# Optimization experiments

Measured on AMD Instinct MI355X. Metric: run time of the kernel, lower is better.

Reference implementation:

```python
import jax, jax.numpy as jnp
import numpy as np

N = 100000   # nodes
E = 600000   # edges
D = 128      # input = hidden = output dim
L = 3        # GNN layers
C = 40       # num_classes
EPS = 1e-5   # BatchNorm eps


def setup_inputs() -> dict:
    key = jax.random.key(0)
    ks = jax.random.split(key, 8)
    x = jax.random.normal(ks[0], (N, D), jnp.float32)
    edge_index = jax.random.randint(ks[1], (2, E), 0, N, jnp.int32)
    # GCNConv weights per layer (Glorot-ish scale), bias zeros
    Ws = jax.random.normal(ks[2], (L, D, D), jnp.float32) / np.sqrt(D)
    bs = jnp.zeros((L, D), jnp.float32)
    # BatchNorm affine params
    gammas = jnp.ones((L, D), jnp.float32)
    betas = jnp.zeros((L, D), jnp.float32)
    # PReLU single slope per layer (torch default init 0.25)
    prelu_a = jnp.full((L,), 0.25, jnp.float32)
    # classification head: Linear(D,D) -> ReLU -> Linear(D,C)
    Wh1 = jax.random.normal(ks[3], (D, D), jnp.float32) / np.sqrt(D)
    bh1 = jnp.zeros((D,), jnp.float32)
    Wh2 = jax.random.normal(ks[4], (D, C), jnp.float32) / np.sqrt(D)
    bh2 = jnp.zeros((C,), jnp.float32)
    return dict(x=x, edge_index=edge_index, Ws=Ws, bs=bs, gammas=gammas,
                betas=betas, prelu_a=prelu_a, Wh1=Wh1, bh1=bh1, Wh2=Wh2, bh2=bh2)


def _gcn_conv(h, src, dst, norm, W, b):
    # PyG GCNConv: out_i = sum_{j->i} norm_ij * (x_j W) + b  (self-loops already in src/dst)
    m = (h @ W)[src] * norm[:, None]          # [E+N, D_out]
    return jax.ops.segment_sum(m, dst, num_segments=N) + b


def reference(x, edge_index, Ws, bs, gammas, betas, prelu_a, Wh1, bh1, Wh2, bh2):
    # add self-loops + symmetric normalization (computed once; same graph each layer)
    loops = jnp.arange(N, dtype=edge_index.dtype)
    src = jnp.concatenate([edge_index[0], loops])
    dst = jnp.concatenate([edge_index[1], loops])
    deg = jax.ops.segment_sum(jnp.ones_like(dst, jnp.float32), dst, num_segments=N)
    dinv = jax.lax.rsqrt(jnp.maximum(deg, 1.0))  # deg >= 1 thanks to self-loops
    norm = dinv[src] * dinv[dst]                 # [E+N]

    h = x
    for l in range(L):
        h = _gcn_conv(h, src, dst, norm, Ws[l], bs[l])
        # BatchNorm in training mode: batch statistics over nodes
        mu = h.mean(axis=0)
        var = h.var(axis=0)
        h = (h - mu) * jax.lax.rsqrt(var + EPS) * gammas[l] + betas[l]
        # PReLU
        h = jnp.where(h > 0, h, prelu_a[l] * h)

    embeddings = h
    logits = jax.nn.relu(embeddings @ Wh1 + bh1) @ Wh2 + bh2
    out = jnp.argmax(logits, axis=1)
    return embeddings, logits, out
```

## Files before the change

### kernel.cpp

```cpp
#include <hip/hip_runtime.h>
#include <hip/hip_bf16.h>
#include <cstddef>

#define N_NODES 100000
#define N_EDGES 600000
#define DD 128
#define LL 3
#define CC 40
#define BN_EPS 1e-5f

typedef __attribute__((ext_vector_type(8))) short bfrag;
typedef __attribute__((ext_vector_type(4))) float f32x4;

__device__ __forceinline__ float ldf(const void* p, long i, int f32) {
    return f32 ? ((const float*)p)[i] : __bfloat162float(((const __hip_bfloat16*)p)[i]);
}
__device__ __forceinline__ void stf(void* p, long i, float v, int f32) {
    if (f32) ((float*)p)[i] = v;
    else     ((__hip_bfloat16*)p)[i] = __float2bfloat16(v);
}

__device__ __forceinline__ unsigned short f2bf(float f) {
    unsigned u = __float_as_uint(f);
    unsigned r = (u + 0x7fffu + ((u >> 16) & 1u)) >> 16;
    return (unsigned short)r;
}
__device__ __forceinline__ float bf2f(unsigned short h) {
    return __uint_as_float(((unsigned)h) << 16);
}

__global__ __launch_bounds__(256) void k_detect(const void* __restrict__ x, int* __restrict__ dflag) {
    __shared__ int s[256];
    int t = threadIdx.x;
    const __hip_bfloat16* xb = (const __hip_bfloat16*)x;
    int bad = 0;
    for (int i = t; i < 4096; i += 256) {
        float v = __bfloat162float(xb[i]);
        float a = fabsf(v);
        if (!(a < 1e6f)) bad++;
        else if (v != 0.f && a < 1e-30f) bad++;
    }
    s[t] = bad; __syncthreads();
    for (int off = 128; off > 0; off >>= 1) {
        if (t < off) s[t] += s[t + off];
        __syncthreads();
    }
    if (t == 0) *dflag = (s[0] > 64) ? 1 : 0;
}

__global__ __launch_bounds__(256) void k_packw(const void* __restrict__ Ws, const void* __restrict__ Wh1,
                                               unsigned short* __restrict__ Wp,
                                               const int* __restrict__ dflag) {
    int f = *dflag;
    int u = blockIdx.x * 256 + threadIdx.x;
    int mat = u >> 14;
    int r = u & 16383;
    int k = r >> 7, c = r & 127;
    float wv = (mat < 3) ? ldf(Ws, (long)mat * 16384 + r, f) : ldf(Wh1, r, f);
    unsigned short hi = f2bf(wv);
    float r1 = wv - bf2f(hi);
    unsigned short mid = f2bf(r1);
    float r2 = r1 - bf2f(mid);
    unsigned short lo = f2bf(r2);
    int n = c >> 4, ks = k >> 5, j = k & 7;
    int lanep = (c & 15) | (((k >> 3) & 3) << 4);
    long base = (long)mat * 49152 + (long)((n * 4 + ks) * 3) * 512 + lanep * 8 + j;
    Wp[base] = hi;
    Wp[base + 512] = mid;
    Wp[base + 1024] = lo;
}


__global__ __launch_bounds__(256) void k_init(int* cnt, int* fpos, int* rowptr, float* stats) {
    int i = blockIdx.x * 256 + threadIdx.x;
    if (i < N_NODES) { cnt[i] = 0; fpos[i] = 0; }
    if (i < 6 * DD) stats[i] = 0.f;
    if (i == 0) rowptr[N_NODES] = N_EDGES;
}

__global__ __launch_bounds__(256) void k_count(const int* __restrict__ ei, int* __restrict__ cnt) {
    int e = blockIdx.x * 256 + threadIdx.x;
    if (e < N_EDGES) atomicAdd(&cnt[ei[N_EDGES + e]], 1);
}

__global__ __launch_bounds__(256) void k_scan1(const int* __restrict__ cnt, int* __restrict__ rowptr,
                                               int* __restrict__ bsum, float* __restrict__ dinv) {
    __shared__ int s[256];
    int t = threadIdx.x;
    int i = blockIdx.x * 256 + t;
    int v = (i < N_NODES) ? cnt[i] : 0;
    if (i < N_NODES) dinv[i] = 1.f / sqrtf((float)(1 + v));
    s[t] = v; __syncthreads();
    for (int off = 1; off < 256; off <<= 1) {
        int x = (t >= off) ? s[t - off] : 0;
        __syncthreads();
        s[t] += x; __syncthreads();
    }
    if (i < N_NODES) rowptr[i] = s[t] - v;
    if (t == 255) bsum[blockIdx.x] = s[255];
}

__global__ __launch_bounds__(512) void k_scan2(int* bsum, int nb) {
    __shared__ int s[512];
    int t = threadIdx.x;
    int v = (t < nb) ? bsum[t] : 0;
    s[t] = v; __syncthreads();
    for (int off = 1; off < 512; off <<= 1) {
        int x = (t >= off) ? s[t - off] : 0;
        __syncthreads();
        s[t] += x; __syncthreads();
    }
    if (t < nb) bsum[t] = s[t] - v;
}

__global__ __launch_bounds__(256) void k_scan3(int* rowptr, const int* __restrict__ bsum) {
    int i = blockIdx.x * 256 + threadIdx.x;
    if (i < N_NODES) rowptr[i] += bsum[blockIdx.x];
}

__global__ __launch_bounds__(256) void k_fill(const int* __restrict__ ei, int* __restrict__ fpos,
                                              const int* __restrict__ rowptr, int* __restrict__ adj,
                                              float* __restrict__ wadj, const float* __restrict__ dinv) {
    int e = blockIdx.x * 256 + threadIdx.x;
    if (e < N_EDGES) {
        int s = ei[e];
        int d = ei[N_EDGES + e];
        int p = atomicAdd(&fpos[d], 1);
        int pos = rowptr[d] + p;
        adj[pos] = s;
        wadj[pos] = dinv[s];
    }
}

__device__ __forceinline__ float4 load_row4(const void* __restrict__ src, long row, int q, int f) {
    if (f) {
        return ((const float4*)src)[row * 32 + q];
    } else {
        uint2 u = ((const uint2*)src)[row * 32 + q];
        float4 v;
        v.x = __uint_as_float(u.x << 16);
        v.y = __uint_as_float(u.x & 0xffff0000u);
        v.z = __uint_as_float(u.y << 16);
        v.w = __uint_as_float(u.y & 0xffff0000u);
        return v;
    }
}


__global__ __launch_bounds__(256) void k_agg(const void* __restrict__ src,
                                             const int* __restrict__ rowptr,
                                             const int* __restrict__ adj,
                                             const float* __restrict__ wadj,
                                             const float* __restrict__ dinv,
                                             const float* __restrict__ bnp,
                                             float* __restrict__ outp,
                                             const int* __restrict__ dflag) {
    int f = *dflag;
    int lane = threadIdx.x & 63;
    int h = lane >> 5;
    int q = lane & 31;
    int i = blockIdx.x * 4 + (threadIdx.x >> 6);
    if (i >= N_NODES) return;

    float4 sc = make_float4(1.f, 1.f, 1.f, 1.f);
    float4 sh = make_float4(0.f, 0.f, 0.f, 0.f);
    float al = 0.f;
    bool useBN = (bnp != nullptr);
    if (useBN) {
        sc = ((const float4*)bnp)[q];
        sh = ((const float4*)(bnp + 128))[q];
        al = bnp[256];
    }

    float di = dinv[i];
    int e0 = rowptr[i], e1 = rowptr[i + 1];

    float a0 = 0.f, a1 = 0.f, a2 = 0.f, a3 = 0.f;
    if (h == 0) {
        float4 v = load_row4(src, i, q, f);
        if (useBN) {
            float y;
            y = fmaf(v.x, sc.x, sh.x); v.x = (y > 0.f) ? y : al * y;
            y = fmaf(v.y, sc.y, sh.y); v.y = (y > 0.f) ? y : al * y;
            y = fmaf(v.z, sc.z, sh.z); v.z = (y > 0.f) ? y : al * y;
            y = fmaf(v.w, sc.w, sh.w); v.w = (y > 0.f) ? y : al * y;
        }
        a0 = di * v.x; a1 = di * v.y; a2 = di * v.z; a3 = di * v.w;
    }

    for (int base = e0; base < e1; base += 64) {
        int m = e1 - base; if (m > 64) m = 64;
        int ajl = (lane < m) ? adj[base + lane] : 0;
        float wl = (lane < m) ? wadj[base + lane] : 0.f;
        for (int t = 0; t < m; t += 4) {
            int s0 = t + h;     if (s0 > 63) s0 = 63;
            int s1 = t + 2 + h; if (s1 > 63) s1 = 63;
            int j0 = __shfl(ajl, s0);
            int j1 = __shfl(ajl, s1);
            float w0 = __shfl(wl, s0);
            float w1 = __shfl(wl, s1);
            float4 v0 = load_row4(src, j0, q, f);
            float4 v1 = load_row4(src, j1, q, f);
            if (useBN) {
                float y;
                y = fmaf(v0.x, sc.x, sh.x); v0.x = (y > 0.f) ? y : al * y;
                y = fmaf(v0.y, sc.y, sh.y); v0.y = (y > 0.f) ? y : al * y;
                y = fmaf(v0.z, sc.z, sh.z); v0.z = (y > 0.f) ? y : al * y;
                y = fmaf(v0.w, sc.w, sh.w); v0.w = (y > 0.f) ? y : al * y;
                y = fmaf(v1.x, sc.x, sh.x); v1.x = (y > 0.f) ? y : al * y;
                y = fmaf(v1.y, sc.y, sh.y); v1.y = (y > 0.f) ? y : al * y;
                y = fmaf(v1.z, sc.z, sh.z); v1.z = (y > 0.f) ? y : al * y;
                y = fmaf(v1.w, sc.w, sh.w); v1.w = (y > 0.f) ? y : al * y;
            }
            a0 += w0 * v0.x + w1 * v1.x;
            a1 += w0 * v0.y + w1 * v1.y;
            a2 += w0 * v0.z + w1 * v1.z;
            a3 += w0 * v0.w + w1 * v1.w;
        }
    }

    a0 += __shfl_xor(a0, 32);
    a1 += __shfl_xor(a1, 32);
    a2 += __shfl_xor(a2, 32);
    a3 += __shfl_xor(a3, 32);

    if (h == 0) {
        float4 r = make_float4(di * a0, di * a1, di * a2, di * a3);
        ((float4*)outp)[(size_t)i * 32 + q] = r;
    }
}


__global__ __launch_bounds__(256, 2) void k_gemm2(const float* __restrict__ A,
                                                  const unsigned short* __restrict__ Wp,
                                                  const void* __restrict__ bias, long boff,
                                                  const float* __restrict__ bnpA,
                                                  float* __restrict__ stats,
                                                  float* __restrict__ Cout, int relu,
                                                  const int* __restrict__ dflag) {
    __shared__ unsigned short Wl[24576];
    int f = *dflag;
    int tid = threadIdx.x;

    int lane = tid & 63;
    int w = tid >> 6;
    int lr = lane & 15;
    int lg = lane >> 4;
    int rowbase = blockIdx.x * 128 + w * 32;

    float bcol[8];
    #pragma unroll
    for (int n = 0; n < 8; ++n)
        bcol[n] = bias ? ldf(bias, boff + n * 16 + lr, f) : 0.f;

    float alA = bnpA ? bnpA[256] : 0.f;

    bfrag ah[2][4], am[2][4], alo[2][4];
    const float4* A4 = (const float4*)A;
    #pragma unroll
    for (int ks = 0; ks < 4; ++ks) {
        int k0 = ks * 32 + lg * 8;
        float bs_[8], bh_[8];
        if (bnpA) {
            float4 sa = *(const float4*)&bnpA[k0];
            float4 sb = *(const float4*)&bnpA[k0 + 4];
            float4 ha = *(const float4*)&bnpA[128 + k0];
            float4 hb = *(const float4*)&bnpA[128 + k0 + 4];
            bs_[0] = sa.x; bs_[1] = sa.y; bs_[2] = sa.z; bs_[3] = sa.w;
            bs_[4] = sb.x; bs_[5] = sb.y; bs_[6] = sb.z; bs_[7] = sb.w;
            bh_[0] = ha.x; bh_[1] = ha.y; bh_[2] = ha.z; bh_[3] = ha.w;
            bh_[4] = hb.x; bh_[5] = hb.y; bh_[6] = hb.z; bh_[7] = hb.w;
        }
        #pragma unroll
        for (int s = 0; s < 2; ++s) {
            int row = rowbase + s * 16 + lr;
            float xv[8];
            if (row < N_NODES) {
                long bi = (long)row * 32 + (k0 >> 2);
                float4 x0 = A4[bi], x1 = A4[bi + 1];
                xv[0] = x0.x; xv[1] = x0.y; xv[2] = x0.z; xv[3] = x0.w;
                xv[4] = x1.x; xv[5] = x1.y; xv[6] = x1.z; xv[7] = x1.w;
            } else {
                #pragma unroll
                for (int e = 0; e < 8; ++e) xv[e] = 0.f;
            }
            if (bnpA) {
                #pragma unroll
                for (int e = 0; e < 8; ++e) {
                    float y = fmaf(xv[e], bs_[e], bh_[e]);
                    xv[e] = (y > 0.f) ? y : alA * y;
                }
            }
            bfrag hfr, mfr, lfr;
            #pragma unroll
            for (int e = 0; e < 8; ++e) {
                unsigned short hb2 = f2bf(xv[e]);
                float r1 = xv[e] - bf2f(hb2);
                unsigned short mb2 = f2bf(r1);
                float r2 = r1 - bf2f(mb2);
                hfr[e] = (short)hb2;
                mfr[e] = (short)mb2;
                lfr[e] = (short)f2bf(r2);
            }
            ah[s][ks] = hfr;
            am[s][ks] = mfr;
            alo[s][ks] = lfr;
        }
    }

    f32x4 acc[2][8];
    #pragma unroll
    for (int s = 0; s < 2; ++s)
        #pragma unroll
        for (int n = 0; n < 8; ++n) acc[s][n] = (f32x4){0.f, 0.f, 0.f, 0.f};

    #pragma unroll
    for (int h = 0; h < 2; ++h) {
        if (h) __syncthreads();
        {
            const uint4* srcp = (const uint4*)(Wp + (size_t)h * 24576);
            uint4* dstp = (uint4*)Wl;
            #pragma unroll
            for (int u = 0; u < 12; ++u) dstp[tid + 256 * u] = srcp[tid + 256 * u];
        }
        __syncthreads();

        #pragma unroll
        for (int nn = 0; nn < 4; ++nn) {
            int n = h * 4 + nn;
            bfrag bh[4], bm[4], bl[4];
            #pragma unroll
            for (int ks = 0; ks < 4; ++ks) {
                int base = ((nn * 4 + ks) * 3) * 512 + lane * 8;
                bh[ks] = *(const bfrag*)&Wl[base];
                bm[ks] = *(const bfrag*)&Wl[base + 512];
                bl[ks] = *(const bfrag*)&Wl[base + 1024];
            }
            #pragma unroll
            for (int ks = 0; ks < 4; ++ks) {
                #pragma unroll
                for (int s = 0; s < 2; ++s) {
                    acc[s][n] = __builtin_amdgcn_mfma_f32_16x16x32_bf16(ah[s][ks],  bh[ks], acc[s][n], 0, 0, 0);
                    acc[s][n] = __builtin_amdgcn_mfma_f32_16x16x32_bf16(am[s][ks],  bh[ks], acc[s][n], 0, 0, 0);
                    acc[s][n] = __builtin_amdgcn_mfma_f32_16x16x32_bf16(ah[s][ks],  bm[ks], acc[s][n], 0, 0, 0);
                    acc[s][n] = __builtin_amdgcn_mfma_f32_16x16x32_bf16(am[s][ks],  bm[ks], acc[s][n], 0, 0, 0);
                    acc[s][n] = __builtin_amdgcn_mfma_f32_16x16x32_bf16(alo[s][ks], bh[ks], acc[s][n], 0, 0, 0);
                    acc[s][n] = __builtin_amdgcn_mfma_f32_16x16x32_bf16(ah[s][ks],  bl[ks], acc[s][n], 0, 0, 0);
                }
            }
        }
    }

    int rowst[2][4]; bool rv[2][4];
    #pragma unroll
    for (int s = 0; s < 2; ++s)
        #pragma unroll
        for (int reg = 0; reg < 4; ++reg) {
            rowst[s][reg] = rowbase + s * 16 + lg * 4 + reg;
            rv[s][reg] = rowst[s][reg] < N_NODES;
        }

    float ls[8], lq[8];
    #pragma unroll
    for (int n = 0; n < 8; ++n) { ls[n] = 0.f; lq[n] = 0.f; }

    #pragma unroll
    for (int s = 0; s < 2; ++s)
        #pragma unroll
        for (int n = 0; n < 8; ++n) {
            int colb = n * 16 + lr;
            #pragma unroll
            for (int reg = 0; reg < 4; ++reg) {
                if (rv[s][reg]) {
                    float o = acc[s][n][reg] + bcol[n];
                    if (relu) o = fmaxf(o, 0.f);
                    Cout[(long)rowst[s][reg] * 128 + colb] = o;
                    ls[n] += o;
                    lq[n] += o * o;
                }
            }
        }

    if (stats) {
        #pragma unroll
        for (int n = 0; n < 8; ++n) {
            ls[n] += __shfl_xor(ls[n], 16);
            ls[n] += __shfl_xor(ls[n], 32);
            lq[n] += __shfl_xor(lq[n], 16);
            lq[n] += __shfl_xor(lq[n], 32);
        }
        __syncthreads();
        float* red = (float*)Wl;
        if (lane < 16) {
            #pragma unroll
            for (int n = 0; n < 8; ++n) {
                red[w * 256 + n * 16 + lane] = ls[n];
                red[w * 256 + 128 + n * 16 + lane] = lq[n];
            }
        }
        __syncthreads();
        float t = red[tid] + red[256 + tid] + red[512 + tid] + red[768 + tid];
        atomicAdd(&stats[tid], t);
    }
}

__global__ __launch_bounds__(128) void k_bnprep(const float* __restrict__ stats,
                                                const void* __restrict__ g, const void* __restrict__ b,
                                                const void* __restrict__ a, int l,
                                                float* __restrict__ bnp, const int* __restrict__ dflag) {
    int f = *dflag;
    int c = threadIdx.x;
    float mean = stats[c] / (float)N_NODES;
    float var = stats[128 + c] / (float)N_NODES - mean * mean;
    float inv = 1.f / sqrtf(var + BN_EPS);
    float s = ldf(g, (long)l * DD + c, f) * inv;
    bnp[c] = s;
    bnp[128 + c] = ldf(b, (long)l * DD + c, f) - mean * s;
    if (c == 0) bnp[256] = ldf(a, l, f);
}

__global__ __launch_bounds__(256) void k_emb(const float* __restrict__ H, const float* __restrict__ bnp,
                                             void* __restrict__ out, const int* __restrict__ dflag) {
    int f = *dflag;
    long idx = (long)blockIdx.x * 256 + threadIdx.x;
    int c = (int)(idx & 127);
    float al = bnp[256];
    float y = fmaf(H[idx], bnp[c], bnp[128 + c]);
    y = (y > 0.f) ? y : al * y;
    stf(out, idx, y, f);
}


__global__ __launch_bounds__(256) void k_head(const float* __restrict__ Hd, const void* __restrict__ W2,
                                              const void* __restrict__ b2,
                                              void* __restrict__ out_base,
                                              const int* __restrict__ dflag) {
    __shared__ float Wl[128][40];
    __shared__ float bl[40];
    __shared__ float rv[32][8];
    __shared__ int ri[32][8];
    int f = *dflag;
    int tid = threadIdx.x;
    for (int u = tid; u < 128 * 40; u += 256) Wl[u / 40][u % 40] = ldf(W2, u, f);
    if (tid < 40) bl[tid] = ldf(b2, tid, f);
    __syncthreads();
    int rl = tid >> 3, g = tid & 7;
    long r = (long)blockIdx.x * 32 + rl;
    float acc[5];
    #pragma unroll
    for (int j = 0; j < 5; ++j) acc[j] = bl[g * 5 + j];
    for (int k = 0; k < 128; ++k) {
        float h = Hd[r * 128 + k];
        #pragma unroll
        for (int j = 0; j < 5; ++j) acc[j] += h * Wl[k][g * 5 + j];
    }
    float best = acc[0]; int bi = 0;
    #pragma unroll
    for (int j = 1; j < 5; ++j)
        if (acc[j] > best) { best = acc[j]; bi = j; }
    const long LOG_OFF = (long)N_NODES * DD;
    const long ARG_OFF = (long)N_NODES * (DD + CC);
    #pragma unroll
    for (int j = 0; j < 5; ++j) stf(out_base, LOG_OFF + r * 40 + g * 5 + j, acc[j], f);
    rv[rl][g] = best; ri[rl][g] = g * 5 + bi;
    __syncthreads();
    if (tid < 32) {
        long row = (long)blockIdx.x * 32 + tid;
        float bb = rv[tid][0]; int bbi = ri[tid][0];
        #pragma unroll
        for (int g2 = 1; g2 < 8; ++g2)
            if (rv[tid][g2] > bb) { bb = rv[tid][g2]; bbi = ri[tid][g2]; }
        stf(out_base, ARG_OFF + row, (float)bbi, f);
    }
}


extern "C" void kernel_launch(void* const* d_in, const int* in_sizes, int n_in,
                              void* d_out, int out_size, void* d_ws, size_t ws_size,
                              hipStream_t stream) {
    const void* x   = d_in[0];
    const int* ei   = (const int*)d_in[1];
    const void* Ws  = d_in[2];
    const void* bs  = d_in[3];
    const void* gam = d_in[4];
    const void* bet = d_in[5];
    const void* pa  = d_in[6];
    const void* Wh1 = d_in[7];
    const void* bh1 = d_in[8];
    const void* Wh2 = d_in[9];
    const void* bh2 = d_in[10];

    char* w = (char*)d_ws;
    int* cnt     = (int*)w;    w += sizeof(int) * N_NODES;
    int* fpos    = (int*)w;    w += sizeof(int) * N_NODES;
    int* rowptr  = (int*)w;    w += sizeof(int) * (N_NODES + 4);
    int* adj     = (int*)w;    w += sizeof(int) * N_EDGES;
    float* wadj  = (float*)w;  w += sizeof(float) * N_EDGES;
    int* bsum    = (int*)w;    w += sizeof(int) * 512;
    int* dflag   = (int*)w;    w += sizeof(int) * 4;
    float* dinv  = (float*)w;  w += sizeof(float) * N_NODES;
    float* stats = (float*)w;  w += sizeof(float) * (6 * DD);
    float* bnp   = (float*)w;  w += sizeof(float) * (3 * 512);
    unsigned short* Wp = (unsigned short*)w; w += sizeof(unsigned short) * 4 * 49152;
    float* bufA  = (float*)w;  w += sizeof(float) * (size_t)N_NODES * DD;
    float* bufB  = (float*)w;  w += sizeof(float) * (size_t)N_NODES * DD;

    const int scanBlocks = (N_NODES + 255) / 256;
    const int edgeBlocks = (N_EDGES + 255) / 256;
    const int elemBlocks = (N_NODES * DD) / 256;
    const int gemmBlocks = (N_NODES + 127) / 128;
    const int aggBlocks  = (N_NODES + 3) / 4;

    k_detect<<<1, 256, 0, stream>>>(x, dflag);
    k_packw<<<256, 256, 0, stream>>>(Ws, Wh1, Wp, dflag);
    k_init<<<scanBlocks, 256, 0, stream>>>(cnt, fpos, rowptr, stats);
    k_count<<<edgeBlocks, 256, 0, stream>>>(ei, cnt);
    k_scan1<<<scanBlocks, 256, 0, stream>>>(cnt, rowptr, bsum, dinv);
    k_scan2<<<1, 512, 0, stream>>>(bsum, scanBlocks);
    k_scan3<<<scanBlocks, 256, 0, stream>>>(rowptr, bsum);
    k_fill<<<edgeBlocks, 256, 0, stream>>>(ei, fpos, rowptr, adj, wadj, dinv);

    for (int l = 0; l < LL; ++l) {
        const void* src = (l == 0) ? x : (const void*)bufB;
        const float* bn = (l == 0) ? nullptr : (bnp + (l - 1) * 512);
        k_agg<<<aggBlocks, 256, 0, stream>>>(src, rowptr, adj, wadj, dinv, bn, bufA, dflag);
        k_gemm2<<<gemmBlocks, 256, 0, stream>>>(bufA, Wp + (size_t)l * 49152, bs, (long)l * DD,
                                                nullptr, stats + l * 256, bufB, 0, dflag);
        k_bnprep<<<1, 128, 0, stream>>>(stats + l * 256, gam, bet, pa, l, bnp + l * 512, dflag);
    }

    k_emb<<<elemBlocks, 256, 0, stream>>>(bufB, bnp + 2 * 512, d_out, dflag);
    k_gemm2<<<gemmBlocks, 256, 0, stream>>>(bufB, Wp + (size_t)3 * 49152, bh1, 0, bnp + 2 * 512,
                                            nullptr, bufA, 1, dflag);
    k_head<<<(N_NODES / 32), 256, 0, stream>>>(bufA, Wh2, bh2, d_out, dflag);
}
```

Measured before the change: 646.2 us.

## Fuse BN prep and embedding write into consumers, interleave adjacency, async weight loads

Removes the k_bnprep and k_emb kernels. BN scale and shift are now recomputed from the stats inside k_agg and k_gemm2, and the embedding output is written from the head GEMM's A-load path. Adjacency indices and weights are interleaved into one int2 array, and the aggregation inner loop is unrolled to four neighbor rows per step for more loads in flight. GEMM weight tiles are loaded with global_load_lds directly into LDS, and the first half is issued before the A-fragment setup. In exchange, every block redoes the per-channel sqrt and division work and carries more register pressure.

New measurement: 641.7 us. No clear change (-0.7%).

```diff
diff --git a/kernel.cpp b/kernel.cpp
--- a/kernel.cpp
+++ b/kernel.cpp
@@ -27,6 +27,11 @@
 }
 __device__ __forceinline__ float bf2f(unsigned short h) {
     return __uint_as_float(((unsigned)h) << 16);
+}
+
+__device__ __forceinline__ void gload_lds16(const unsigned short* g, unsigned short* l) {
+    __builtin_amdgcn_global_load_lds((const __attribute__((address_space(1))) unsigned int*)g,
+                                     (__attribute__((address_space(3))) unsigned int*)l, 16, 0, 0);
 }
 
 __global__ __launch_bounds__(256) void k_detect(const void* __restrict__ x, int* __restrict__ dflag) {
@@ -119,16 +124,14 @@
 }
 
 __global__ __launch_bounds__(256) void k_fill(const int* __restrict__ ei, int* __restrict__ fpos,
-                                              const int* __restrict__ rowptr, int* __restrict__ adj,
-                                              float* __restrict__ wadj, const float* __restrict__ dinv) {
+                                              const int* __restrict__ rowptr, int2* __restrict__ adjw,
+                                              const float* __restrict__ dinv) {
     int e = blockIdx.x * 256 + threadIdx.x;
     if (e < N_EDGES) {
         int s = ei[e];
         int d = ei[N_EDGES + e];
         int p = atomicAdd(&fpos[d], 1);
-        int pos = rowptr[d] + p;
-        adj[pos] = s;
-        wadj[pos] = dinv[s];
+        adjw[rowptr[d] + p] = make_int2(s, __float_as_int(dinv[s]));
     }
 }
 
@@ -146,13 +149,25 @@
     }
 }
 
+__device__ __forceinline__ float4 bn4(float4 v, float4 sc, float4 sh, float al) {
+    float y;
+    y = fmaf(v.x, sc.x, sh.x); v.x = (y > 0.f) ? y : al * y;
+    y = fmaf(v.y, sc.y, sh.y); v.y = (y > 0.f) ? y : al * y;
+    y = fmaf(v.z, sc.z, sh.z); v.z = (y > 0.f) ? y : al * y;
+    y = fmaf(v.w, sc.w, sh.w); v.w = (y > 0.f) ? y : al * y;
+    return v;
+}
+
 
 __global__ __launch_bounds__(256) void k_agg(const void* __restrict__ src,
                                              const int* __restrict__ rowptr,
-                                             const int* __restrict__ adj,
-                                             const float* __restrict__ wadj,
+                                             const int2* __restrict__ adjw,
                                              const float* __restrict__ dinv,
-                                             const float* __restrict__ bnp,
+                                             const float* __restrict__ stats,
+                                             const void* __restrict__ gam,
+                                             const void* __restrict__ bet,
+                                             const void* __restrict__ pa,
+                                             int bnl,
                                              float* __restrict__ outp,
                                              const int* __restrict__ dflag) {
     int f = *dflag;
@@ -162,14 +177,25 @@
     int i = blockIdx.x * 4 + (threadIdx.x >> 6);
     if (i >= N_NODES) return;
 
+    bool useBN = (stats != nullptr);
     float4 sc = make_float4(1.f, 1.f, 1.f, 1.f);
     float4 sh = make_float4(0.f, 0.f, 0.f, 0.f);
     float al = 0.f;
-    bool useBN = (bnp != nullptr);
     if (useBN) {
-        sc = ((const float4*)bnp)[q];
-        sh = ((const float4*)(bnp + 128))[q];
-        al = bnp[256];
+        const float invn = 1.f / (float)N_NODES;
+        float4 sm = ((const float4*)stats)[q];
+        float4 sq = ((const float4*)(stats + 128))[q];
+        long gb = (long)bnl * DD + 4 * q;
+        float m0 = sm.x * invn, m1 = sm.y * invn, m2 = sm.z * invn, m3 = sm.w * invn;
+        sc.x = ldf(gam, gb + 0, f) / sqrtf(sq.x * invn - m0 * m0 + BN_EPS);
+        sc.y = ldf(gam, gb + 1, f) / sqrtf(sq.y * invn - m1 * m1 + BN_EPS);
+        sc.z = ldf(gam, gb + 2, f) / sqrtf(sq.z * invn - m2 * m2 + BN_EPS);
+        sc.w = ldf(gam, gb + 3, f) / sqrtf(sq.w * invn - m3 * m3 + BN_EPS);
+        sh.x = ldf(bet, gb + 0, f) - m0 * sc.x;
+        sh.y = ldf(bet, gb + 1, f) - m1 * sc.y;
+        sh.z = ldf(bet, gb + 2, f) - m2 * sc.z;
+        sh.w = ldf(bet, gb + 3, f) - m3 * sc.w;
+        al = ldf(pa, bnl, f);
     }
 
     float di = dinv[i];
@@ -178,44 +204,37 @@
     float a0 = 0.f, a1 = 0.f, a2 = 0.f, a3 = 0.f;
     if (h == 0) {
         float4 v = load_row4(src, i, q, f);
-        if (useBN) {
-            float y;
-            y = fmaf(v.x, sc.x, sh.x); v.x = (y > 0.f) ? y : al * y;
-            y = fmaf(v.y, sc.y, sh.y); v.y = (y > 0.f) ? y : al * y;
-            y = fmaf(v.z, sc.z, sh.z); v.z = (y > 0.f) ? y : al * y;
-            y = fmaf(v.w, sc.w, sh.w); v.w = (y > 0.f) ? y : al * y;
-        }
+        if (useBN) v = bn4(v, sc, sh, al);
         a0 = di * v.x; a1 = di * v.y; a2 = di * v.z; a3 = di * v.w;
     }
 
     for (int base = e0; base < e1; base += 64) {
         int m = e1 - base; if (m > 64) m = 64;
-        int ajl = (lane < m) ? adj[base + lane] : 0;
-        float wl = (lane < m) ? wadj[base + lane] : 0.f;
-        for (int t = 0; t < m; t += 4) {
-            int s0 = t + h;     if (s0 > 63) s0 = 63;
-            int s1 = t + 2 + h; if (s1 > 63) s1 = 63;
-            int j0 = __shfl(ajl, s0);
-            int j1 = __shfl(ajl, s1);
-            float w0 = __shfl(wl, s0);
-            float w1 = __shfl(wl, s1);
-            float4 v0 = load_row4(src, j0, q, f);
-            float4 v1 = load_row4(src, j1, q, f);
+        int2 aw = (lane < m) ? adjw[base + lane] : make_int2(0, 0);
+        int ajl = aw.x;
+        float wl = __int_as_float(aw.y);
+        for (int t = 0; t < m; t += 8) {
+            int jj[4]; float ww[4];
+            #pragma unroll
+            for (int u = 0; u < 4; ++u) {
+                int s = t + 2 * u + h; if (s > 63) s = 63;
+                jj[u] = __shfl(ajl, s);
+                ww[u] = __shfl(wl, s);
+            }
+            float4 v0 = load_row4(src, jj[0], q, f);
+            float4 v1 = load_row4(src, jj[1], q, f);
+            float4 v2 = load_row4(src, jj[2], q, f);
+            float4 v3 = load_row4(src, jj[3], q, f);
             if (useBN) {
-                float y;
-                y = fmaf(v0.x, sc.x, sh.x); v0.x = (y > 0.f) ? y : al * y;
-                y = fmaf(v0.y, sc.y, sh.y); v0.y = (y > 0.f) ? y : al * y;
-                y = fmaf(v0.z, sc.z, sh.z); v0.z = (y > 0.f) ? y : al * y;
-                y = fmaf(v0.w, sc.w, sh.w); v0.w = (y > 0.f) ? y : al * y;
-                y = fmaf(v1.x, sc.x, sh.x); v1.x = (y > 0.f) ? y : al * y;
-                y = fmaf(v1.y, sc.y, sh.y); v1.y = (y > 0.f) ? y : al * y;
-                y = fmaf(v1.z, sc.z, sh.z); v1.z = (y > 0.f) ? y : al * y;
-                y = fmaf(v1.w, sc.w, sh.w); v1.w = (y > 0.f) ? y : al * y;
-            }
-            a0 += w0 * v0.x + w1 * v1.x;
-            a1 += w0 * v0.y + w1 * v1.y;
-            a2 += w0 * v0.z + w1 * v1.z;
-            a3 += w0 * v0.w + w1 * v1.w;
+                v0 = bn4(v0, sc, sh, al);
+                v1 = bn4(v1, sc, sh, al);
+                v2 = bn4(v2, sc, sh, al);
+                v3 = bn4(v3, sc, sh, al);
+            }
+            a0 += ww[0] * v0.x + ww[1] * v1.x + ww[2] * v2.x + ww[3] * v3.x;
+            a1 += ww[0] * v0.y + ww[1] * v1.y + ww[2] * v2.y + ww[3] * v3.y;
+            a2 += ww[0] * v0.z + ww[1] * v1.z + ww[2] * v2.z + ww[3] * v3.z;
+            a3 += ww[0] * v0.w + ww[1] * v1.w + ww[2] * v2.w + ww[3] * v3.w;
         }
     }
 
@@ -234,16 +253,26 @@
 __global__ __launch_bounds__(256, 2) void k_gemm2(const float* __restrict__ A,
                                                   const unsigned short* __restrict__ Wp,
                                                   const void* __restrict__ bias, long boff,
-                                                  const float* __restrict__ bnpA,
+                                                  const float* __restrict__ statsA,
+                                                  const void* __restrict__ gam,
+                                                  const void* __restrict__ bet,
+                                                  const void* __restrict__ pa, int bnl,
                                                   float* __restrict__ stats,
-                                                  float* __restrict__ Cout, int relu,
+                                                  float* __restrict__ Cout,
+                                                  void* __restrict__ embp, int relu,
                                                   const int* __restrict__ dflag) {
     __shared__ unsigned short Wl[24576];
     int f = *dflag;
     int tid = threadIdx.x;
-
     int lane = tid & 63;
     int w = tid >> 6;
+
+    #pragma unroll
+    for (int u = 0; u < 12; ++u) {
+        int chunk = w * 12 + u;
+        gload_lds16(Wp + chunk * 512 + lane * 8, &Wl[chunk * 512]);
+    }
+
     int lr = lane & 15;
     int lg = lane >> 4;
     int rowbase = blockIdx.x * 128 + w * 32;
@@ -253,7 +282,8 @@
     for (int n = 0; n < 8; ++n)
         bcol[n] = bias ? ldf(bias, boff + n * 16 + lr, f) : 0.f;
 
-    float alA = bnpA ? bnpA[256] : 0.f;
+    float alA = statsA ? ldf(pa, bnl, f) : 0.f;
+    const float invn = 1.f / (float)N_NODES;
 
     bfrag ah[2][4], am[2][4], alo[2][4];
     const float4* A4 = (const float4*)A;
@@ -261,15 +291,16 @@
     for (int ks = 0; ks < 4; ++ks) {
         int k0 = ks * 32 + lg * 8;
         float bs_[8], bh_[8];
-        if (bnpA) {
-            float4 sa = *(const float4*)&bnpA[k0];
-            float4 sb = *(const float4*)&bnpA[k0 + 4];
-            float4 ha = *(const float4*)&bnpA[128 + k0];
-            float4 hb = *(const float4*)&bnpA[128 + k0 + 4];
-            bs_[0] = sa.x; bs_[1] = sa.y; bs_[2] = sa.z; bs_[3] = sa.w;
-            bs_[4] = sb.x; bs_[5] = sb.y; bs_[6] = sb.z; bs_[7] = sb.w;
-            bh_[0] = ha.x; bh_[1] = ha.y; bh_[2] = ha.z; bh_[3] = ha.w;
-            bh_[4] = hb.x; bh_[5] = hb.y; bh_[6] = hb.z; bh_[7] = hb.w;
+        if (statsA) {
+            #pragma unroll
+            for (int e = 0; e < 8; ++e) {
+                int c = k0 + e;
+                float mean = statsA[c] * invn;
+                float varv = statsA[128 + c] * invn - mean * mean;
+                float s = ldf(gam, (long)bnl * DD + c, f) / sqrtf(varv + BN_EPS);
+                bs_[e] = s;
+                bh_[e] = ldf(bet, (long)bnl * DD + c, f) - mean * s;
+            }
         }
         #pragma unroll
         for (int s = 0; s < 2; ++s) {
@@ -284,7 +315,7 @@
                 #pragma unroll
                 for (int e = 0; e < 8; ++e) xv[e] = 0.f;
             }
-            if (bnpA) {
+            if (statsA) {
                 #pragma unroll
                 for (int e = 0; e < 8; ++e) {
                     float y = fmaf(xv[e], bs_[e], bh_[e]);
@@ -305,6 +336,19 @@
             ah[s][ks] = hfr;
             am[s][ks] = mfr;
             alo[s][ks] = lfr;
+            if (embp && row < N_NODES) {
+                if (f) {
+                    ((float4*)embp)[(long)row * 32 + (k0 >> 2)]     = make_float4(xv[0], xv[1], xv[2], xv[3]);
+                    ((float4*)embp)[(long)row * 32 + (k0 >> 2) + 1] = make_float4(xv[4], xv[5], xv[6], xv[7]);
+                } else {
+                    uint4 pk;
+                    pk.x = (unsigned)(unsigned short)hfr[0] | ((unsigned)(unsigned short)hfr[1] << 16);
+                    pk.y = (unsigned)(unsigned short)hfr[2] | ((unsigned)(unsigned short)hfr[3] << 16);
+                    pk.z = (unsigned)(unsigned short)hfr[4] | ((unsigned)(unsigned short)hfr[5] << 16);
+                    pk.w = (unsigned)(unsigned short)hfr[6] | ((unsigned)(unsigned short)hfr[7] << 16);
+                    ((uint4*)embp)[(long)row * 16 + (k0 >> 3)] = pk;
+                }
+            }
         }
     }
 
@@ -314,39 +358,62 @@
         #pragma unroll
         for (int n = 0; n < 8; ++n) acc[s][n] = (f32x4){0.f, 0.f, 0.f, 0.f};
 
-    #pragma unroll
-    for (int h = 0; h < 2; ++h) {
-        if (h) __syncthreads();
-        {
-            const uint4* srcp = (const uint4*)(Wp + (size_t)h * 24576);
-            uint4* dstp = (uint4*)Wl;
-            #pragma unroll
-            for (int u = 0; u < 12; ++u) dstp[tid + 256 * u] = srcp[tid + 256 * u];
-        }
-        __syncthreads();
-
-        #pragma unroll
-        for (int nn = 0; nn < 4; ++nn) {
-            int n = h * 4 + nn;
-            bfrag bh[4], bm[4], bl[4];
-            #pragma unroll
-            for (int ks = 0; ks < 4; ++ks) {
-                int base = ((nn * 4 + ks) * 3) * 512 + lane * 8;
-                bh[ks] = *(const bfrag*)&Wl[base];
-                bm[ks] = *(const bfrag*)&Wl[base + 512];
-                bl[ks] = *(const bfrag*)&Wl[base + 1024];
-            }
-            #pragma unroll
-            for (int ks = 0; ks < 4; ++ks) {
-                #pragma unroll
-                for (int s = 0; s < 2; ++s) {
-                    acc[s][n] = __builtin_amdgcn_mfma_f32_16x16x32_bf16(ah[s][ks],  bh[ks], acc[s][n], 0, 0, 0);
-                    acc[s][n] = __builtin_amdgcn_mfma_f32_16x16x32_bf16(am[s][ks],  bh[ks], acc[s][n], 0, 0, 0);
-                    acc[s][n] = __builtin_amdgcn_mfma_f32_16x16x32_bf16(ah[s][ks],  bm[ks], acc[s][n], 0, 0, 0);
-                    acc[s][n] = __builtin_amdgcn_mfma_f32_16x16x32_bf16(am[s][ks],  bm[ks], acc[s][n], 0, 0, 0);
-                    acc[s][n] = __builtin_amdgcn_mfma_f32_16x16x32_bf16(alo[s][ks], bh[ks], acc[s][n], 0, 0, 0);
-                    acc[s][n] = __builtin_amdgcn_mfma_f32_16x16x32_bf16(ah[s][ks],  bl[ks], acc[s][n], 0, 0, 0);
-                }
+    __syncthreads();
+
+    #pragma unroll
+    for (int nn = 0; nn < 4; ++nn) {
+        int n = nn;
+        bfrag bh[4], bm[4], bl[4];
+        #pragma unroll
+        for (int ks = 0; ks < 4; ++ks) {
+            int base = ((nn * 4 + ks) * 3) * 512 + lane * 8;
+            bh[ks] = *(const bfrag*)&Wl[base];
+            bm[ks] = *(const bfrag*)&Wl[base + 512];
+            bl[ks] = *(const bfrag*)&Wl[base + 1024];
+        }
+        #pragma unroll
+        for (int ks = 0; ks < 4; ++ks) {
+            #pragma unroll
+            for (int s = 0; s < 2; ++s) {
+                acc[s][n] = __builtin_amdgcn_mfma_f32_16x16x32_bf16(ah[s][ks],  bh[ks], acc[s][n], 0, 0, 0);
+                acc[s][n] = __builtin_amdgcn_mfma_f32_16x16x32_bf16(am[s][ks],  bh[ks], acc[s][n], 0, 0, 0);
+                acc[s][n] = __builtin_amdgcn_mfma_f32_16x16x32_bf16(ah[s][ks],  bm[ks], acc[s][n], 0, 0, 0);
+                acc[s][n] = __builtin_amdgcn_mfma_f32_16x16x32_bf16(am[s][ks],  bm[ks], acc[s][n], 0, 0, 0);
+                acc[s][n] = __builtin_amdgcn_mfma_f32_16x16x32_bf16(alo[s][ks], bh[ks], acc[s][n], 0, 0, 0);
+                acc[s][n] = __builtin_amdgcn_mfma_f32_16x16x32_bf16(ah[s][ks],  bl[ks], acc[s][n], 0, 0, 0);
+            }
+        }
+    }
+
+    __syncthreads();
+    #pragma unroll
+    for (int u = 0; u < 12; ++u) {
+        int chunk = w * 12 + u;
+        gload_lds16(Wp + 24576 + chunk * 512 + lane * 8, &Wl[chunk * 512]);
+    }
+    __syncthreads();
+
+    #pragma unroll
+    for (int nn = 0; nn < 4; ++nn) {
+        int n = 4 + nn;
+        bfrag bh[4], bm[4], bl[4];
+        #pragma unroll
+        for (int ks = 0; ks < 4; ++ks) {
+            int base = ((nn * 4 + ks) * 3) * 512 + lane * 8;
+            bh[ks] = *(const bfrag*)&Wl[base];
+            bm[ks] = *(const bfrag*)&Wl[base + 512];
+            bl[ks] = *(const bfrag*)&Wl[base + 1024];
+        }
+        #pragma unroll
+        for (int ks = 0; ks < 4; ++ks) {
+            #pragma unroll
+            for (int s = 0; s < 2; ++s) {
+                acc[s][n] = __builtin_amdgcn_mfma_f32_16x16x32_bf16(ah[s][ks],  bh[ks], acc[s][n], 0, 0, 0);
+                acc[s][n] = __builtin_amdgcn_mfma_f32_16x16x32_bf16(am[s][ks],  bh[ks], acc[s][n], 0, 0, 0);
+                acc[s][n] = __builtin_amdgcn_mfma_f32_16x16x32_bf16(ah[s][ks],  bm[ks], acc[s][n], 0, 0, 0);
+                acc[s][n] = __builtin_amdgcn_mfma_f32_16x16x32_bf16(am[s][ks],  bm[ks], acc[s][n], 0, 0, 0);
+                acc[s][n] = __builtin_amdgcn_mfma_f32_16x16x32_bf16(alo[s][ks], bh[ks], acc[s][n], 0, 0, 0);
+                acc[s][n] = __builtin_amdgcn_mfma_f32_16x16x32_bf16(ah[s][ks],  bl[ks], acc[s][n], 0, 0, 0);
             }
         }
     }
@@ -402,32 +469,6 @@
         float t = red[tid] + red[256 + tid] + red[512 + tid] + red[768 + tid];
         atomicAdd(&stats[tid], t);
     }
-}
-
-__global__ __launch_bounds__(128) void k_bnprep(const float* __restrict__ stats,
-                                                const void* __restrict__ g, const void* __restrict__ b,
-                                                const void* __restrict__ a, int l,
-                                                float* __restrict__ bnp, const int* __restrict__ dflag) {
-    int f = *dflag;
-    int c = threadIdx.x;
-    float mean = stats[c] / (float)N_NODES;
-    float var = stats[128 + c] / (float)N_NODES - mean * mean;
-    float inv = 1.f / sqrtf(var + BN_EPS);
-    float s = ldf(g, (long)l * DD + c, f) * inv;
-    bnp[c] = s;
-    bnp[128 + c] = ldf(b, (long)l * DD + c, f) - mean * s;
-    if (c == 0) bnp[256] = ldf(a, l, f);
-}
-
-__global__ __launch_bounds__(256) void k_emb(const float* __restrict__ H, const float* __restrict__ bnp,
-                                             void* __restrict__ out, const int* __restrict__ dflag) {
-    int f = *dflag;
-    long idx = (long)blockIdx.x * 256 + threadIdx.x;
-    int c = (int)(idx & 127);
-    float al = bnp[256];
-    float y = fmaf(H[idx], bnp[c], bnp[128 + c]);
-    y = (y > 0.f) ? y : al * y;
-    stf(out, idx, y, f);
 }
 
 
@@ -494,20 +535,17 @@
     int* cnt     = (int*)w;    w += sizeof(int) * N_NODES;
     int* fpos    = (int*)w;    w += sizeof(int) * N_NODES;
     int* rowptr  = (int*)w;    w += sizeof(int) * (N_NODES + 4);
-    int* adj     = (int*)w;    w += sizeof(int) * N_EDGES;
-    float* wadj  = (float*)w;  w += sizeof(float) * N_EDGES;
+    int2* adjw   = (int2*)w;   w += sizeof(int2) * N_EDGES;
     int* bsum    = (int*)w;    w += sizeof(int) * 512;
     int* dflag   = (int*)w;    w += sizeof(int) * 4;
     float* dinv  = (float*)w;  w += sizeof(float) * N_NODES;
     float* stats = (float*)w;  w += sizeof(float) * (6 * DD);
-    float* bnp   = (float*)w;  w += sizeof(float) * (3 * 512);
     unsigned short* Wp = (unsigned short*)w; w += sizeof(unsigned short) * 4 * 49152;
     float* bufA  = (float*)w;  w += sizeof(float) * (size_t)N_NODES * DD;
     float* bufB  = (float*)w;  w += sizeof(float) * (size_t)N_NODES * DD;
 
     const int scanBlocks = (N_NODES + 255) / 256;
     const int edgeBlocks = (N_EDGES + 255) / 256;
-    const int elemBlocks = (N_NODES * DD) / 256;
     const int gemmBlocks = (N_NODES + 127) / 128;
     const int aggBlocks  = (N_NODES + 3) / 4;
 
@@ -518,19 +556,20 @@
     k_scan1<<<scanBlocks, 256, 0, stream>>>(cnt, rowptr, bsum, dinv);
     k_scan2<<<1, 512, 0, stream>>>(bsum, scanBlocks);
     k_scan3<<<scanBlocks, 256, 0, stream>>>(rowptr, bsum);
-    k_fill<<<edgeBlocks, 256, 0, stream>>>(ei, fpos, rowptr, adj, wadj, dinv);
+    k_fill<<<edgeBlocks, 256, 0, stream>>>(ei, fpos, rowptr, adjw, dinv);
 
     for (int l = 0; l < LL; ++l) {
         const void* src = (l == 0) ? x : (const void*)bufB;
-        const float* bn = (l == 0) ? nullptr : (bnp + (l - 1) * 512);
-        k_agg<<<aggBlocks, 256, 0, stream>>>(src, rowptr, adj, wadj, dinv, bn, bufA, dflag);
+        const float* st = (l == 0) ? nullptr : (stats + (l - 1) * 256);
+        k_agg<<<aggBlocks, 256, 0, stream>>>(src, rowptr, adjw, dinv, st, gam, bet, pa,
+                                             l - 1, bufA, dflag);
         k_gemm2<<<gemmBlocks, 256, 0, stream>>>(bufA, Wp + (size_t)l * 49152, bs, (long)l * DD,
-                                                nullptr, stats + l * 256, bufB, 0, dflag);
-        k_bnprep<<<1, 128, 0, stream>>>(stats + l * 256, gam, bet, pa, l, bnp + l * 512, dflag);
-    }
-
-    k_emb<<<elemBlocks, 256, 0, stream>>>(bufB, bnp + 2 * 512, d_out, dflag);
-    k_gemm2<<<gemmBlocks, 256, 0, stream>>>(bufB, Wp + (size_t)3 * 49152, bh1, 0, bnp + 2 * 512,
-                                            nullptr, bufA, 1, dflag);
+                                                nullptr, gam, bet, pa, 0,
+                                                stats + l * 256, bufB, nullptr, 0, dflag);
+    }
+
+    k_gemm2<<<gemmBlocks, 256, 0, stream>>>(bufB, Wp + (size_t)3 * 49152, bh1, 0,
+                                            stats + 2 * 256, gam, bet, pa, 2,
+                                            nullptr, bufA, d_out, 1, dflag);
     k_head<<<(N_NODES / 32), 256, 0, stream>>>(bufA, Wh2, bh2, d_out, dflag);
 }
```
